# Kernel optimization log

Hardware: AMD Instinct MI355X
Metric: run time of the kernel (lower is better)

The kernel has to match this reference:

```python
import jax, jax.numpy as jnp
import numpy as np

BSZ = 64
SEQ = 64      # logits rows per sequence (cu_seqlens_q stride)
CAND = 32     # candidates per batch == block_size
VOCAB = 32000
TOTAL = BSZ * CAND


def setup_inputs() -> dict:
    key = jax.random.key(0)
    k1, k2, k3, k4, k5 = jax.random.split(key, 5)
    input_logits = jax.random.normal(k1, (BSZ * SEQ, VOCAB), dtype=jnp.float32)
    relative_idx = jax.random.randint(k2, (TOTAL,), 0, SEQ, dtype=jnp.int32)
    batch_offsets = jnp.arange(BSZ, dtype=jnp.int32) * SEQ
    cu_filtered = jnp.arange(BSZ + 1, dtype=jnp.int32) * CAND
    cu_seqlens_q = jnp.arange(BSZ + 1, dtype=jnp.int32) * SEQ
    temperatures = 0.5 + 1.5 * jax.random.uniform(k3, (TOTAL,), dtype=jnp.float32)
    num_transfer = jax.random.randint(k4, (BSZ,), 0, 16, dtype=jnp.int32)
    thresholds = 0.3 * jax.random.uniform(k5, (BSZ,), dtype=jnp.float32)
    top_p = jnp.full((1,), 0.9, dtype=jnp.float32)
    return {
        'input_logits': input_logits, 'relative_idx': relative_idx,
        'batch_offsets': batch_offsets, 'cu_filtered': cu_filtered,
        'cu_seqlens_q': cu_seqlens_q, 'temperatures': temperatures,
        'num_transfer': num_transfer, 'thresholds': thresholds,
        'top_p': top_p, 'top_k': 50, 'block_size': CAND,
    }


def reference(input_logits, relative_idx, batch_offsets, cu_filtered, cu_seqlens_q,
              temperatures, num_transfer, thresholds, top_p, top_k, block_size):
    bsz = cu_filtered.shape[0] - 1
    total = relative_idx.shape[0]
    vocab = input_logits.shape[-1]
    NEG = jnp.finfo(input_logits.dtype).min

    # triton_repeat_interleave: group id of each candidate token
    counts = cu_filtered[1:] - cu_filtered[:-1]                      # [B]
    group_ids = jnp.repeat(jnp.arange(bsz), counts, total_repeat_length=total)
    k_values = jnp.maximum(num_transfer, 0)

    # gather candidate logits rows
    global_rows = cu_seqlens_q[:-1][group_ids] + relative_idx        # [T]
    cand = jnp.take(input_logits, global_rows, axis=0)               # [T, V]
    scaled = cand / temperatures[:, None]

    # top_k_logits
    kk = min(int(top_k), vocab)
    topk_vals = jax.lax.top_k(scaled, kk)[0]                         # [T, kk]
    thr_k = topk_vals[:, kk - 1][:, None]
    scaled = jnp.where(scaled < thr_k, NEG, scaled)

    # top_p_logits (nucleus)
    order = jnp.argsort(-scaled, axis=-1)                            # descending
    sorted_logits = jnp.take_along_axis(scaled, order, axis=-1)
    cum = jnp.cumsum(jax.nn.softmax(sorted_logits, axis=-1), axis=-1)
    remove = cum > top_p.reshape(-1, 1)
    remove = jnp.concatenate([jnp.zeros_like(remove[:, :1]), remove[:, :-1]], axis=-1)
    inv = jnp.argsort(order, axis=-1)                                # inverse permutation
    mask = jnp.take_along_axis(remove, inv, axis=-1)
    scaled = jnp.where(mask, NEG, scaled)

    probs = jax.nn.softmax(scaled, axis=-1)
    top_probs = probs.max(axis=-1)                                   # scores ('confidence')
    top_tokens = probs.argmax(axis=-1).astype(jnp.int32)             # greedy sample_token
    abs_idx = relative_idx + batch_offsets[group_ids]

    # ragged_to_dense: [B, block_size], padded with -inf / 0 / 0
    pos_in_row = jnp.arange(block_size)[None, :]                     # [1, L]
    row_mask = pos_in_row < counts[:, None]                          # [B, L]
    flat = jnp.where(row_mask, cu_filtered[:-1, None] + pos_in_row, 0)
    dense_scores = jnp.where(row_mask, top_probs[flat], -jnp.inf)
    dense_tokens = jnp.where(row_mask, top_tokens[flat], 0)
    dense_pos = jnp.where(row_mask, abs_idx[flat], 0)

    # per-row descending sort by score (padding -inf sorts last)
    sort_idx = jnp.argsort(-dense_scores, axis=1)
    sorted_scores = jnp.take_along_axis(dense_scores, sort_idx, axis=1)
    sorted_tokens = jnp.take_along_axis(dense_tokens, sort_idx, axis=1)
    sorted_pos = jnp.take_along_axis(dense_pos, sort_idx, axis=1)

    # filter_and_count
    keep = (pos_in_row < k_values[:, None]) \
        & (sorted_scores >= thresholds[:, None]) \
        & (sorted_scores > -jnp.inf)
    out_tokens = jnp.where(keep, sorted_tokens, -1)
    out_pos = jnp.where(keep, sorted_pos, 0)
    out_counts = keep.sum(axis=1).astype(jnp.int32)
    return out_pos, out_tokens, out_counts
```

## Files before the change

### kernel.cpp

```cpp
#include <hip/hip_runtime.h>
#include <math.h>

#define THREADS 256
#define CAP 512
#define HIST_BINS 4096
#define RAW_THRESH 2.5f

__device__ __forceinline__ unsigned orderKey(float f) {
    unsigned u = __float_as_uint(f);
    return (u & 0x80000000u) ? ~u : (u | 0x80000000u);
}

union SmemU {
    struct { float vals[CAP]; int idx[CAP]; float sorted[CAP]; } a;
    int hist[HIST_BINS];
};

__global__ __launch_bounds__(THREADS, 8) void token_kernel(
    const float* __restrict__ logits,
    const int* __restrict__ rel_idx,
    const int* __restrict__ cu_filtered,
    const int* __restrict__ cu_q,
    const float* __restrict__ temps,
    const int* __restrict__ topk_p,
    const float* __restrict__ topp_p,
    int bsz, long long logits_n,
    float* __restrict__ ws_prob,
    int* __restrict__ ws_token)
{
    __shared__ SmemU u;
    __shared__ int s_n, s_m, s_amax;
    __shared__ unsigned s_T, s_maxkey;

    const int t = blockIdx.x;
    const int tid = threadIdx.x;

    if (tid == 0) s_n = 0;

    int lo = 0, hi = bsz;
    while (hi - lo > 1) {
        int mid = (lo + hi) >> 1;
        if (t >= cu_filtered[mid]) lo = mid; else hi = mid;
    }
    const int b = lo;

    const int nrows = cu_q[bsz];
    const int vocab = (int)(logits_n / (long long)nrows);
    int kk = topk_p[0];
    if (kk > vocab) kk = vocab;
    const float T = temps[t];
    const long long grow = (long long)cu_q[b] + (long long)rel_idx[t];
    const float* row = logits + grow * (long long)vocab;
    const float4* row4 = (const float4*)row;
    const int nv4 = vocab >> 2;
    __syncthreads();

    int i = tid;
    for (; i + THREADS < nv4; i += 2 * THREADS) {
        float4 v0 = row4[i];
        float4 v1 = row4[i + THREADS];
        int b0 = i << 2, b1 = (i + THREADS) << 2;
        if (v0.x >= RAW_THRESH) { int p = atomicAdd(&s_n, 1); if (p < CAP) { u.a.vals[p] = v0.x / T; u.a.idx[p] = b0; } }
        if (v0.y >= RAW_THRESH) { int p = atomicAdd(&s_n, 1); if (p < CAP) { u.a.vals[p] = v0.y / T; u.a.idx[p] = b0 + 1; } }
        if (v0.z >= RAW_THRESH) { int p = atomicAdd(&s_n, 1); if (p < CAP) { u.a.vals[p] = v0.z / T; u.a.idx[p] = b0 + 2; } }
        if (v0.w >= RAW_THRESH) { int p = atomicAdd(&s_n, 1); if (p < CAP) { u.a.vals[p] = v0.w / T; u.a.idx[p] = b0 + 3; } }
        if (v1.x >= RAW_THRESH) { int p = atomicAdd(&s_n, 1); if (p < CAP) { u.a.vals[p] = v1.x / T; u.a.idx[p] = b1; } }
        if (v1.y >= RAW_THRESH) { int p = atomicAdd(&s_n, 1); if (p < CAP) { u.a.vals[p] = v1.y / T; u.a.idx[p] = b1 + 1; } }
        if (v1.z >= RAW_THRESH) { int p = atomicAdd(&s_n, 1); if (p < CAP) { u.a.vals[p] = v1.z / T; u.a.idx[p] = b1 + 2; } }
        if (v1.w >= RAW_THRESH) { int p = atomicAdd(&s_n, 1); if (p < CAP) { u.a.vals[p] = v1.w / T; u.a.idx[p] = b1 + 3; } }
    }
    for (; i < nv4; i += THREADS) {
        float4 v = row4[i];
        int base = i << 2;
        if (v.x >= RAW_THRESH) { int p = atomicAdd(&s_n, 1); if (p < CAP) { u.a.vals[p] = v.x / T; u.a.idx[p] = base; } }
        if (v.y >= RAW_THRESH) { int p = atomicAdd(&s_n, 1); if (p < CAP) { u.a.vals[p] = v.y / T; u.a.idx[p] = base + 1; } }
        if (v.z >= RAW_THRESH) { int p = atomicAdd(&s_n, 1); if (p < CAP) { u.a.vals[p] = v.z / T; u.a.idx[p] = base + 2; } }
        if (v.w >= RAW_THRESH) { int p = atomicAdd(&s_n, 1); if (p < CAP) { u.a.vals[p] = v.w / T; u.a.idx[p] = base + 3; } }
    }
    for (int j = (nv4 << 2) + tid; j < vocab; j += THREADS) {
        float v = row[j];
        if (v >= RAW_THRESH) { int p = atomicAdd(&s_n, 1); if (p < CAP) { u.a.vals[p] = v / T; u.a.idx[p] = j; } }
    }
    __syncthreads();
    int n = s_n;

    if (n < kk || n > CAP) {
        __syncthreads();
        for (int j = tid; j < HIST_BINS; j += THREADS) u.hist[j] = 0;
        if (tid == 0) { s_n = 0; s_maxkey = 0; }
        __syncthreads();
        for (int j = tid; j < vocab; j += THREADS) {
            float a = row[j] / T;
            unsigned k = orderKey(a);
            atomicAdd(&u.hist[k >> 20], 1);
            atomicMax(&s_maxkey, k);
        }
        __syncthreads();
        if (tid == 0) {
            int B = (int)(s_maxkey >> 20);
            int cum = 0;
            while (true) {
                cum += u.hist[B];
                if (cum >= kk || B == 0) break;
                --B;
            }
            s_T = ((unsigned)B) << 20;
        }
        __syncthreads();
        const unsigned Tkey = s_T;
        for (int j = tid; j < vocab; j += THREADS) {
            float a = row[j] / T;
            if (orderKey(a) >= Tkey) {
                int p = atomicAdd(&s_n, 1);
                if (p < CAP) { u.a.vals[p] = a; u.a.idx[p] = j; }
            }
        }
        __syncthreads();
        n = s_n;
        if (n > CAP) n = CAP;
    }

    for (int j = tid; j < n; j += THREADS) {
        float v = u.a.vals[j];
        int id = u.a.idx[j];
        int r = 0;
        for (int q = 0; q < n; ++q) {
            float w = u.a.vals[q];
            r += (w > v) || (w == v && u.a.idx[q] < id);
        }
        u.a.sorted[r] = v;
        if (r == 0) s_amax = id;
    }
    __syncthreads();

    if (tid == 0) {
        float thr = u.a.sorted[kk - 1];
        int m = kk;
        while (m < n && u.a.sorted[m] >= thr) ++m;
        s_m = m;
    }
    __syncthreads();
    const int m = s_m;
    const float M = u.a.sorted[0];
    for (int j = tid; j < m; j += THREADS) u.a.vals[j] = expf(u.a.sorted[j] - M);
    __syncthreads();
    if (tid == 0) {
        float Z1 = 0.f;
        for (int j = 0; j < m; ++j) Z1 += u.a.vals[j];
        const float topp = topp_p[0];
        int jcut = m - 1;
        float c = 0.f;
        for (int j = 0; j < m; ++j) {
            float p = u.a.vals[j] / Z1;
            c += p;
            if (c > topp) { jcut = j; break; }
        }
        float Z2 = 0.f;
        for (int j = 0; j <= jcut; ++j) Z2 += u.a.vals[j];
        ws_prob[t] = 1.0f / Z2;
        ws_token[t] = s_amax;
    }
}

__global__ __launch_bounds__(64) void finalize_kernel(
    const float* __restrict__ ws_prob,
    const int* __restrict__ ws_token,
    const int* __restrict__ rel_idx,
    const int* __restrict__ boff,
    const int* __restrict__ cu_filtered,
    const int* __restrict__ num_transfer,
    const float* __restrict__ thresholds,
    int bsz, int L,
    int* __restrict__ out)
{
    const int bq = blockIdx.x;
    const int l = threadIdx.x;
    const int start = cu_filtered[bq];
    int cnt = cu_filtered[bq + 1] - start;
    if (cnt > L) cnt = L;

    __shared__ float ss[64]; __shared__ int stk[64]; __shared__ int sp[64];
    __shared__ float ss2[64]; __shared__ int stk2[64]; __shared__ int sp2[64];

    float score = -INFINITY; int tok = 0; int pos = 0;
    if (l < L) {
        if (l < cnt) {
            int t = start + l;
            score = ws_prob[t];
            tok = ws_token[t];
            pos = rel_idx[t] + boff[bq];
        }
        ss[l] = score; stk[l] = tok; sp[l] = pos;
    }
    __syncthreads();
    if (l < L) {
        int r = 0;
        for (int j = 0; j < L; ++j) {
            float w = ss[j];
            r += (w > score) || (w == score && j < l);
        }
        ss2[r] = score; stk2[r] = tok; sp2[r] = pos;
    }
    __syncthreads();

    int k = num_transfer[bq]; if (k < 0) k = 0;
    const float thrb = thresholds[bq];
    bool kp = false;
    if (l < L) {
        float s = ss2[l];
        kp = (l < k) && (s >= thrb) && (s > -INFINITY);
        out[bq * L + l] = kp ? sp2[l] : 0;
        out[bsz * L + bq * L + l] = kp ? stk2[l] : -1;
    }
    unsigned long long mask = __ballot(kp);
    if (l == 0) out[2 * bsz * L + bq] = (int)__popcll(mask);
}

extern "C" void kernel_launch(void* const* d_in, const int* in_sizes, int n_in,
                              void* d_out, int out_size, void* d_ws, size_t ws_size,
                              hipStream_t stream) {
    const float* logits   = (const float*)d_in[0];
    const int*   rel      = (const int*)d_in[1];
    const int*   boff     = (const int*)d_in[2];
    const int*   cuf      = (const int*)d_in[3];
    const int*   cuq      = (const int*)d_in[4];
    const float* temps    = (const float*)d_in[5];
    const int*   ntr      = (const int*)d_in[6];
    const float* thr      = (const float*)d_in[7];
    const float* topp     = (const float*)d_in[8];
    const int*   topk     = (const int*)d_in[9];

    const int total = in_sizes[1];
    const int bsz   = in_sizes[6];
    const long long logits_n = (long long)in_sizes[0];
    const int L = (out_size - bsz) / (2 * bsz);

    float* ws_prob = (float*)d_ws;
    int*   ws_tok  = (int*)(ws_prob + total);

    token_kernel<<<total, THREADS, 0, stream>>>(
        logits, rel, cuf, cuq, temps, topk, topp, bsz, logits_n, ws_prob, ws_tok);

    finalize_kernel<<<bsz, 64, 0, stream>>>(
        ws_prob, ws_tok, rel, boff, cuf, ntr, thr, bsz, L, (int*)d_out);
}
```

Baseline: 76.78 us.

## Deduplicate row processing by sorting each unique logits row once

Splits the work into a per-row kernel that scans each needed logits row once, collects and ranks top candidates on raw logits, and stores them in workspace. A new per-candidate kernel applies temperature, top-k and top-p to the cached sorted list. This relies on temperature scaling preserving order, and avoids re-reading shared rows from HBM. In exchange it adds a launch, workspace traffic, and a per-row scan of rel_idx to skip unused rows.

```diff
diff --git a/kernel.cpp b/kernel.cpp
--- a/kernel.cpp
+++ b/kernel.cpp
@@ -11,186 +11,249 @@
     return (u & 0x80000000u) ? ~u : (u | 0x80000000u);
 }
 
-union SmemU {
-    struct { float vals[CAP]; int idx[CAP]; float sorted[CAP]; } a;
-    int hist[HIST_BINS];
-};
-
-__global__ __launch_bounds__(THREADS, 8) void token_kernel(
+__device__ __forceinline__ void ws_layout(void* ws, int nrows, int total,
+                                          float** svals, int** sidx, int** wsn,
+                                          float** prob, int** tok) {
+    float* f = (float*)ws;
+    *svals = f;
+    *sidx  = (int*)(f + (size_t)nrows * CAP);
+    *wsn   = *sidx + (size_t)nrows * CAP;
+    *prob  = (float*)(*wsn + nrows);
+    *tok   = (int*)(*prob + total);
+}
+
+#define COLLECT1(x, gi) \
+    if ((x) >= RAW_THRESH) { int p = atomicAdd(&s_n, 1); if (p < CAP) { u.a.v[p] = (x); u.a.id[p] = (gi); } }
+#define COLLECT4(vv, base) \
+    COLLECT1((vv).x, (base)) COLLECT1((vv).y, (base) + 1) \
+    COLLECT1((vv).z, (base) + 2) COLLECT1((vv).w, (base) + 3)
+
+__global__ __launch_bounds__(THREADS, 8) void row_kernel(
     const float* __restrict__ logits,
     const int* __restrict__ rel_idx,
-    const int* __restrict__ cu_filtered,
-    const int* __restrict__ cu_q,
+    const int* __restrict__ cuf,
+    const int* __restrict__ cuq,
+    const int* __restrict__ topk_p,
+    int bsz, int total, long long logits_n, void* ws)
+{
+    __shared__ union {
+        struct { float v[CAP]; int id[CAP]; float sv[CAP]; int si[CAP]; } a;
+        int hist[HIST_BINS];
+    } u;
+    __shared__ int s_n, s_needed;
+    __shared__ unsigned s_T, s_maxkey;
+
+    const int tid = threadIdx.x;
+    const int nrows = cuq[bsz];
+    const int vocab = (int)(logits_n / (long long)nrows);
+    int kk = topk_p[0];
+    if (kk > vocab) kk = vocab;
+
+    float* svals; int* sidx; int* wsn; float* prob; int* tok;
+    ws_layout(ws, nrows, total, &svals, &sidx, &wsn, &prob, &tok);
+
+    for (int r = blockIdx.x; r < nrows; r += gridDim.x) {
+        int lo = 0, hi = bsz;
+        while (hi - lo > 1) { int mid = (lo + hi) >> 1; if (r >= cuq[mid]) lo = mid; else hi = mid; }
+        const int b = lo;
+        const int rel = r - cuq[b];
+
+        if (tid == 0) { s_needed = 0; s_n = 0; }
+        __syncthreads();
+        const int t0 = cuf[b], cnt = cuf[b + 1] - t0;
+        for (int l = tid; l < cnt; l += THREADS)
+            if (rel_idx[t0 + l] == rel) s_needed = 1;
+        __syncthreads();
+        if (!s_needed) continue;
+
+        const float* row = logits + (long long)r * (long long)vocab;
+        const float4* row4 = (const float4*)row;
+        const int nv4 = vocab >> 2;
+
+        int i = tid;
+        for (; i + 3 * THREADS < nv4; i += 4 * THREADS) {
+            float4 v0 = row4[i];
+            float4 v1 = row4[i + THREADS];
+            float4 v2 = row4[i + 2 * THREADS];
+            float4 v3 = row4[i + 3 * THREADS];
+            COLLECT4(v0, i << 2)
+            COLLECT4(v1, (i + THREADS) << 2)
+            COLLECT4(v2, (i + 2 * THREADS) << 2)
+            COLLECT4(v3, (i + 3 * THREADS) << 2)
+        }
+        for (; i < nv4; i += THREADS) {
+            float4 v = row4[i];
+            COLLECT4(v, i << 2)
+        }
+        for (int j = (nv4 << 2) + tid; j < vocab; j += THREADS) {
+            float x = row[j];
+            COLLECT1(x, j)
+        }
+        __syncthreads();
+        int n = s_n;
+
+        if (n < kk || n > CAP) {
+            __syncthreads();
+            for (int j = tid; j < HIST_BINS; j += THREADS) u.hist[j] = 0;
+            if (tid == 0) { s_n = 0; s_maxkey = 0; }
+            __syncthreads();
+            for (int j = tid; j < vocab; j += THREADS) {
+                unsigned k = orderKey(row[j]);
+                atomicAdd(&u.hist[k >> 20], 1);
+                atomicMax(&s_maxkey, k);
+            }
+            __syncthreads();
+            if (tid == 0) {
+                int B = (int)(s_maxkey >> 20);
+                int cum = 0;
+                while (true) {
+                    cum += u.hist[B];
+                    if (cum >= kk || B == 0) break;
+                    --B;
+                }
+                s_T = ((unsigned)B) << 20;
+            }
+            __syncthreads();
+            const unsigned Tk = s_T;
+            for (int j = tid; j < vocab; j += THREADS) {
+                float a = row[j];
+                if (orderKey(a) >= Tk) {
+                    int p = atomicAdd(&s_n, 1);
+                    if (p < CAP) { u.a.v[p] = a; u.a.id[p] = j; }
+                }
+            }
+            __syncthreads();
+            n = s_n;
+            if (n > CAP) n = CAP;
+        }
+
+        for (int j = tid; j < n; j += THREADS) {
+            float v = u.a.v[j];
+            int id = u.a.id[j];
+            int rk = 0;
+            for (int q = 0; q < n; ++q) {
+                float w = u.a.v[q];
+                rk += (w > v) || (w == v && u.a.id[q] < id);
+            }
+            u.a.sv[rk] = v;
+            u.a.si[rk] = id;
+        }
+        __syncthreads();
+        for (int j = tid; j < n; j += THREADS) {
+            svals[(size_t)r * CAP + j] = u.a.sv[j];
+            sidx[(size_t)r * CAP + j]  = u.a.si[j];
+        }
+        if (tid == 0) wsn[r] = n;
+        __syncthreads();
+    }
+}
+
+__global__ __launch_bounds__(64) void token_kernel(
+    const int* __restrict__ rel_idx,
+    const int* __restrict__ cuf,
+    const int* __restrict__ cuq,
     const float* __restrict__ temps,
     const int* __restrict__ topk_p,
     const float* __restrict__ topp_p,
-    int bsz, long long logits_n,
-    float* __restrict__ ws_prob,
-    int* __restrict__ ws_token)
+    int bsz, int total, long long logits_n, void* ws)
 {
-    __shared__ SmemU u;
-    __shared__ int s_n, s_m, s_amax;
-    __shared__ unsigned s_T, s_maxkey;
+    __shared__ float sc[CAP];
+    __shared__ float e[CAP];
+    __shared__ int si[CAP];
+    __shared__ int s_m, s_amax;
 
     const int t = blockIdx.x;
-    const int tid = threadIdx.x;
-
-    if (tid == 0) s_n = 0;
-
-    int lo = 0, hi = bsz;
-    while (hi - lo > 1) {
-        int mid = (lo + hi) >> 1;
-        if (t >= cu_filtered[mid]) lo = mid; else hi = mid;
-    }
-    const int b = lo;
-
-    const int nrows = cu_q[bsz];
+    const int l = threadIdx.x;
+    const int nrows = cuq[bsz];
     const int vocab = (int)(logits_n / (long long)nrows);
     int kk = topk_p[0];
     if (kk > vocab) kk = vocab;
+
+    float* svals; int* sidx; int* wsn; float* prob; int* tok;
+    ws_layout(ws, nrows, total, &svals, &sidx, &wsn, &prob, &tok);
+
+    int lo = 0, hi = bsz;
+    while (hi - lo > 1) { int mid = (lo + hi) >> 1; if (t >= cuf[mid]) lo = mid; else hi = mid; }
+    const int b = lo;
+    const int row = cuq[b] + rel_idx[t];
     const float T = temps[t];
-    const long long grow = (long long)cu_q[b] + (long long)rel_idx[t];
-    const float* row = logits + grow * (long long)vocab;
-    const float4* row4 = (const float4*)row;
-    const int nv4 = vocab >> 2;
-    __syncthreads();
-
-    int i = tid;
-    for (; i + THREADS < nv4; i += 2 * THREADS) {
-        float4 v0 = row4[i];
-        float4 v1 = row4[i + THREADS];
-        int b0 = i << 2, b1 = (i + THREADS) << 2;
-        if (v0.x >= RAW_THRESH) { int p = atomicAdd(&s_n, 1); if (p < CAP) { u.a.vals[p] = v0.x / T; u.a.idx[p] = b0; } }
-        if (v0.y >= RAW_THRESH) { int p = atomicAdd(&s_n, 1); if (p < CAP) { u.a.vals[p] = v0.y / T; u.a.idx[p] = b0 + 1; } }
-        if (v0.z >= RAW_THRESH) { int p = atomicAdd(&s_n, 1); if (p < CAP) { u.a.vals[p] = v0.z / T; u.a.idx[p] = b0 + 2; } }
-        if (v0.w >= RAW_THRESH) { int p = atomicAdd(&s_n, 1); if (p < CAP) { u.a.vals[p] = v0.w / T; u.a.idx[p] = b0 + 3; } }
-        if (v1.x >= RAW_THRESH) { int p = atomicAdd(&s_n, 1); if (p < CAP) { u.a.vals[p] = v1.x / T; u.a.idx[p] = b1; } }
-        if (v1.y >= RAW_THRESH) { int p = atomicAdd(&s_n, 1); if (p < CAP) { u.a.vals[p] = v1.y / T; u.a.idx[p] = b1 + 1; } }
-        if (v1.z >= RAW_THRESH) { int p = atomicAdd(&s_n, 1); if (p < CAP) { u.a.vals[p] = v1.z / T; u.a.idx[p] = b1 + 2; } }
-        if (v1.w >= RAW_THRESH) { int p = atomicAdd(&s_n, 1); if (p < CAP) { u.a.vals[p] = v1.w / T; u.a.idx[p] = b1 + 3; } }
-    }
-    for (; i < nv4; i += THREADS) {
-        float4 v = row4[i];
-        int base = i << 2;
-        if (v.x >= RAW_THRESH) { int p = atomicAdd(&s_n, 1); if (p < CAP) { u.a.vals[p] = v.x / T; u.a.idx[p] = base; } }
-        if (v.y >= RAW_THRESH) { int p = atomicAdd(&s_n, 1); if (p < CAP) { u.a.vals[p] = v.y / T; u.a.idx[p] = base + 1; } }
-        if (v.z >= RAW_THRESH) { int p = atomicAdd(&s_n, 1); if (p < CAP) { u.a.vals[p] = v.z / T; u.a.idx[p] = base + 2; } }
-        if (v.w >= RAW_THRESH) { int p = atomicAdd(&s_n, 1); if (p < CAP) { u.a.vals[p] = v.w / T; u.a.idx[p] = base + 3; } }
-    }
-    for (int j = (nv4 << 2) + tid; j < vocab; j += THREADS) {
-        float v = row[j];
-        if (v >= RAW_THRESH) { int p = atomicAdd(&s_n, 1); if (p < CAP) { u.a.vals[p] = v / T; u.a.idx[p] = j; } }
-    }
-    __syncthreads();
-    int n = s_n;
-
-    if (n < kk || n > CAP) {
-        __syncthreads();
-        for (int j = tid; j < HIST_BINS; j += THREADS) u.hist[j] = 0;
-        if (tid == 0) { s_n = 0; s_maxkey = 0; }
-        __syncthreads();
-        for (int j = tid; j < vocab; j += THREADS) {
-            float a = row[j] / T;
-            unsigned k = orderKey(a);
-            atomicAdd(&u.hist[k >> 20], 1);
-            atomicMax(&s_maxkey, k);
-        }
-        __syncthreads();
-        if (tid == 0) {
-            int B = (int)(s_maxkey >> 20);
-            int cum = 0;
-            while (true) {
-                cum += u.hist[B];
-                if (cum >= kk || B == 0) break;
-                --B;
-            }
-            s_T = ((unsigned)B) << 20;
-        }
-        __syncthreads();
-        const unsigned Tkey = s_T;
-        for (int j = tid; j < vocab; j += THREADS) {
-            float a = row[j] / T;
-            if (orderKey(a) >= Tkey) {
-                int p = atomicAdd(&s_n, 1);
-                if (p < CAP) { u.a.vals[p] = a; u.a.idx[p] = j; }
-            }
-        }
-        __syncthreads();
-        n = s_n;
-        if (n > CAP) n = CAP;
-    }
-
-    for (int j = tid; j < n; j += THREADS) {
-        float v = u.a.vals[j];
-        int id = u.a.idx[j];
-        int r = 0;
-        for (int q = 0; q < n; ++q) {
-            float w = u.a.vals[q];
-            r += (w > v) || (w == v && u.a.idx[q] < id);
-        }
-        u.a.sorted[r] = v;
-        if (r == 0) s_amax = id;
-    }
-    __syncthreads();
-
-    if (tid == 0) {
-        float thr = u.a.sorted[kk - 1];
-        int m = kk;
-        while (m < n && u.a.sorted[m] >= thr) ++m;
-        s_m = m;
-    }
+    const int n = wsn[row];
+
+    for (int j = l; j < n; j += 64) {
+        sc[j] = svals[(size_t)row * CAP + j] / T;
+        si[j] = sidx[(size_t)row * CAP + j];
+    }
+    __syncthreads();
+    const float M = sc[0];
+    const float thrk = sc[kk - 1];
+
+    int mcnt = 0;
+    int cand = 0x7fffffff;
+    for (int j = l; j < n; j += 64) {
+        mcnt += (sc[j] >= thrk) ? 1 : 0;
+        if (sc[j] == M && si[j] < cand) cand = si[j];
+    }
+    for (int off = 32; off > 0; off >>= 1) {
+        mcnt += __shfl_down(mcnt, off);
+        int oc = __shfl_down(cand, off);
+        if (oc < cand) cand = oc;
+    }
+    if (l == 0) { s_m = mcnt; s_amax = cand; }
     __syncthreads();
     const int m = s_m;
-    const float M = u.a.sorted[0];
-    for (int j = tid; j < m; j += THREADS) u.a.vals[j] = expf(u.a.sorted[j] - M);
-    __syncthreads();
-    if (tid == 0) {
+    for (int j = l; j < m; j += 64) e[j] = expf(sc[j] - M);
+    __syncthreads();
+    if (l == 0) {
         float Z1 = 0.f;
-        for (int j = 0; j < m; ++j) Z1 += u.a.vals[j];
+        for (int j = 0; j < m; ++j) Z1 += e[j];
         const float topp = topp_p[0];
         int jcut = m - 1;
         float c = 0.f;
         for (int j = 0; j < m; ++j) {
-            float p = u.a.vals[j] / Z1;
+            float p = e[j] / Z1;
             c += p;
             if (c > topp) { jcut = j; break; }
         }
         float Z2 = 0.f;
-        for (int j = 0; j <= jcut; ++j) Z2 += u.a.vals[j];
-        ws_prob[t] = 1.0f / Z2;
-        ws_token[t] = s_amax;
+        for (int j = 0; j <= jcut; ++j) Z2 += e[j];
+        prob[t] = 1.0f / Z2;
+        tok[t] = s_amax;
     }
 }
 
 __global__ __launch_bounds__(64) void finalize_kernel(
-    const float* __restrict__ ws_prob,
-    const int* __restrict__ ws_token,
     const int* __restrict__ rel_idx,
     const int* __restrict__ boff,
-    const int* __restrict__ cu_filtered,
+    const int* __restrict__ cuf,
+    const int* __restrict__ cuq,
     const int* __restrict__ num_transfer,
     const float* __restrict__ thresholds,
-    int bsz, int L,
+    int bsz, int total, int L,
+    void* ws,
     int* __restrict__ out)
 {
     const int bq = blockIdx.x;
     const int l = threadIdx.x;
-    const int start = cu_filtered[bq];
-    int cnt = cu_filtered[bq + 1] - start;
+    const int nrows = cuq[bsz];
+    float* svals; int* sidx; int* wsn; float* prob; int* tok;
+    ws_layout(ws, nrows, total, &svals, &sidx, &wsn, &prob, &tok);
+
+    const int start = cuf[bq];
+    int cnt = cuf[bq + 1] - start;
     if (cnt > L) cnt = L;
 
     __shared__ float ss[64]; __shared__ int stk[64]; __shared__ int sp[64];
     __shared__ float ss2[64]; __shared__ int stk2[64]; __shared__ int sp2[64];
 
-    float score = -INFINITY; int tok = 0; int pos = 0;
+    float score = -INFINITY; int tk = 0; int pos = 0;
     if (l < L) {
         if (l < cnt) {
             int t = start + l;
-            score = ws_prob[t];
-            tok = ws_token[t];
+            score = prob[t];
+            tk = tok[t];
             pos = rel_idx[t] + boff[bq];
         }
-        ss[l] = score; stk[l] = tok; sp[l] = pos;
+        ss[l] = score; stk[l] = tk; sp[l] = pos;
     }
     __syncthreads();
     if (l < L) {
@@ -199,7 +262,7 @@
             float w = ss[j];
             r += (w > score) || (w == score && j < l);
         }
-        ss2[r] = score; stk2[r] = tok; sp2[r] = pos;
+        ss2[r] = score; stk2[r] = tk; sp2[r] = pos;
     }
     __syncthreads();
 
@@ -235,12 +298,12 @@
     const long long logits_n = (long long)in_sizes[0];
     const int L = (out_size - bsz) / (2 * bsz);
 
-    float* ws_prob = (float*)d_ws;
-    int*   ws_tok  = (int*)(ws_prob + total);
-
-    token_kernel<<<total, THREADS, 0, stream>>>(
-        logits, rel, cuf, cuq, temps, topk, topp, bsz, logits_n, ws_prob, ws_tok);
+    row_kernel<<<total, THREADS, 0, stream>>>(
+        logits, rel, cuf, cuq, topk, bsz, total, logits_n, d_ws);
+
+    token_kernel<<<total, 64, 0, stream>>>(
+        rel, cuf, cuq, temps, topk, topp, bsz, total, logits_n, d_ws);
 
     finalize_kernel<<<bsz, 64, 0, stream>>>(
-        ws_prob, ws_tok, rel, boff, cuf, ntr, thr, bsz, L, (int*)d_out);
-}
+        rel, boff, cuf, cuq, ntr, thr, bsz, total, L, d_ws, (int*)d_out);
+}
```

New measurement: 107.0 us. 39.3% more time.
